# Kernel tuning notes

Hardware: AMD Instinct MI355X
Metric: run time of the kernel (lower is better)

The kernel has to match this reference:

```python
import jax, jax.numpy as jnp
import numpy as np

# ---- fixed configuration (see shape_source) ----
B, ND, NPR = 64, 32, 32          # batch, drug-subgraph nodes, protein-subgraph nodes
LD, LP = 100, 1000               # drug_MAX_LENGH, protein_MAX_LENGH
DIM, CONV = 64, 40               # char_dim, conv
DK, PK = (4, 6, 8), (4, 8, 12)   # drug_kernel, protein_kernel
VD, VP = 71, 26                  # SMILES / FASTA vocab sizes
ED, EP, EDP = 128, 128, 64       # DDI / PPI / DPI edges per subgraph
GNN_LAYERS = 2
SLOPE = 0.01                     # LeakyReLU default slope


def setup_inputs():
    key = jax.random.key(0)
    ks = iter(jax.random.split(key, 64))
    def nrm(shape, s=0.02):
        return jax.random.normal(next(ks), shape, jnp.float32) * s
    inp = {}
    inp['drug_tokens'] = jax.random.randint(next(ks), (B, LD), 0, VD, jnp.int32)
    inp['protein_tokens'] = jax.random.randint(next(ks), (B, LP), 0, VP, jnp.int32)
    inp['drug_node_tokens'] = jax.random.randint(next(ks), (B, ND, LD), 0, VD, jnp.int32)
    inp['protein_node_tokens'] = jax.random.randint(next(ks), (B, NPR, LP), 0, VP, jnp.int32)
    inp['ddi_edges'] = jax.random.randint(next(ks), (B, 2, ED), 0, ND, jnp.int32)
    inp['ppi_edges'] = jax.random.randint(next(ks), (B, 2, EP), 0, NPR, jnp.int32)
    inp['dpi_edges'] = jax.random.randint(next(ks), (B, 2, EDP), 0, min(ND, NPR), jnp.int32)
    # sequence embeddings (padding_idx=0 -> zero row)
    inp['drug_embed'] = nrm((VD, DIM)).at[0].set(0.)
    inp['protein_embed'] = nrm((VP, DIM)).at[0].set(0.)
    # drug CNN stack
    inp['dW1'], inp['db1'] = nrm((CONV, DIM, DK[0])), jnp.zeros((CONV,), jnp.float32)
    inp['dW2'], inp['db2'] = nrm((2*CONV, CONV, DK[1])), jnp.zeros((2*CONV,), jnp.float32)
    inp['dW3'], inp['db3'] = nrm((4*CONV, 2*CONV, DK[2])), jnp.zeros((4*CONV,), jnp.float32)
    # protein CNN stack
    inp['pW1'], inp['pb1'] = nrm((CONV, DIM, PK[0])), jnp.zeros((CONV,), jnp.float32)
    inp['pW2'], inp['pb2'] = nrm((2*CONV, CONV, PK[1])), jnp.zeros((2*CONV,), jnp.float32)
    inp['pW3'], inp['pb3'] = nrm((4*CONV, 2*CONV, PK[2])), jnp.zeros((4*CONV,), jnp.float32)
    # graph node-feature embedding tables (creat_drug_node / creat_protein_node)
    inp['drug_node_table'] = nrm((VD, LD)).at[0].set(0.)
    inp['protein_node_table'] = nrm((VP, LP)).at[0].set(0.)
    # SAGEConv params: Wl (neighbor path, has bias), Wr (root path, no bias)
    inp['ddi_Wl'], inp['ddi_bl'], inp['ddi_Wr'] = nrm((LD, LD)), jnp.zeros((LD,), jnp.float32), nrm((LD, LD))
    inp['ppi_Wl'], inp['ppi_bl'], inp['ppi_Wr'] = nrm((LP, LP)), jnp.zeros((LP,), jnp.float32), nrm((LP, LP))
    inp['dpi_Wl'], inp['dpi_bl'], inp['dpi_Wr'] = nrm((LP, LD)), jnp.zeros((LP,), jnp.float32), nrm((LP, LP))
    inp['pdi_Wl'], inp['pdi_bl'], inp['pdi_Wr'] = nrm((LD, LP)), jnp.zeros((LD,), jnp.float32), nrm((LD, LD))
    # fusion MLP
    inp['fc1_W'], inp['fc1_b'] = nrm((1024, 1420)), jnp.zeros((1024,), jnp.float32)
    inp['fc2_W'], inp['fc2_b'] = nrm((1024, 1024)), jnp.zeros((1024,), jnp.float32)
    inp['fc3_W'], inp['fc3_b'] = nrm((512, 1024)), jnp.zeros((512,), jnp.float32)
    inp['out_W'], inp['out_b'] = nrm((2, 512)), jnp.zeros((2,), jnp.float32)
    return inp


def _conv_relu(x, w, b):
    # x: [B, Cin, L], w: [Cout, Cin, K] -> valid Conv1d + ReLU
    y = jax.lax.conv_general_dilated(x, w, (1,), 'VALID',
                                     dimension_numbers=('NCH', 'OIH', 'NCH'))
    return jax.nn.relu(y + b[None, :, None])


def _node_feat(tokens, table, vocab):
    # mean over sequence of embedded tokens == (token-count histogram / L) @ table
    counts = jax.nn.one_hot(tokens, vocab, dtype=table.dtype).sum(axis=2)  # [B, N, V]
    return jnp.einsum('bnv,vd->bnd', counts, table) / tokens.shape[-1]


def _sage(xs, xd, edges, Wl, bl, Wr):
    # PyG SAGEConv, aggr='mean': lin_l(mean_j x_src[j]) + lin_r(x_dst)
    src, dst = edges[0], edges[1]
    n = xd.shape[0]
    s = jax.ops.segment_sum(xs[src], dst, num_segments=n)
    c = jax.ops.segment_sum(jnp.ones((src.shape[0],), xs.dtype), dst, num_segments=n)
    agg = s / jnp.maximum(c, 1.0)[:, None]
    return agg @ Wl.T + bl + xd @ Wr.T


def _forward(drug_tokens, protein_tokens, drug_node_tokens, protein_node_tokens,
             ddi_edges, ppi_edges, dpi_edges,
             drug_embed, protein_embed,
             dW1, db1, dW2, db2, dW3, db3,
             pW1, pb1, pW2, pb2, pW3, pb3,
             drug_node_table, protein_node_table,
             ddi_Wl, ddi_bl, ddi_Wr, ppi_Wl, ppi_bl, ppi_Wr,
             dpi_Wl, dpi_bl, dpi_Wr, pdi_Wl, pdi_bl, pdi_Wr,
             fc1_W, fc1_b, fc2_W, fc2_b, fc3_W, fc3_b, out_W, out_b):
    # --- CNN branches (maxpool kernel spans whole remaining length == global max) ---
    x = drug_embed[drug_tokens].transpose(0, 2, 1)            # [B, DIM, LD]
    for w, b in ((dW1, db1), (dW2, db2), (dW3, db3)):
        x = _conv_relu(x, w, b)
    drug_feat = x.max(axis=2)                                 # [B, 4*CONV]
    y = protein_embed[protein_tokens].transpose(0, 2, 1)      # [B, DIM, LP]
    for w, b in ((pW1, pb1), (pW2, pb2), (pW3, pb3)):
        y = _conv_relu(y, w, b)
    prot_feat = y.max(axis=2)                                 # [B, 4*CONV]
    # --- graph node features: mean over sequence of node-token embeddings ---
    dx = _node_feat(drug_node_tokens, drug_node_table, VD)    # [B, ND, LD]
    px = _node_feat(protein_node_tokens, protein_node_table, VP)  # [B, NPR, LP]
    # --- hetero SAGE message passing, aggr='mean' across relations ---
    def _hetero(dxi, pxi, ddi, ppi, dpi):
        pdi = dpi[::-1]
        d = 0.5 * (_sage(dxi, dxi, ddi, ddi_Wl, ddi_bl, ddi_Wr)
                   + _sage(pxi, dxi, pdi, pdi_Wl, pdi_bl, pdi_Wr))
        p = 0.5 * (_sage(pxi, pxi, ppi, ppi_Wl, ppi_bl, ppi_Wr)
                   + _sage(dxi, pxi, dpi, dpi_Wl, dpi_bl, dpi_Wr))
        return d, p
    hetero_b = jax.vmap(_hetero)
    for _ in range(GNN_LAYERS):
        dx, px = hetero_b(dx, px, ddi_edges, ppi_edges, dpi_edges)
    # node 0 of each subgraph is the query drug / protein
    graph_feat = jnp.concatenate([dx[:, 0], px[:, 0]], axis=-1)   # [B, LD+LP]
    # --- fusion MLP (dropout = identity at eval) ---
    pair = jnp.concatenate([drug_feat, prot_feat, graph_feat], axis=-1)  # [B, 1420]
    h = jax.nn.leaky_relu(pair @ fc1_W.T + fc1_b, SLOPE)
    h = jax.nn.leaky_relu(h @ fc2_W.T + fc2_b, SLOPE)
    h = jax.nn.leaky_relu(h @ fc3_W.T + fc3_b, SLOPE)
    return h @ out_W.T + out_b                                 # [B, 2]


def reference(drug_tokens, protein_tokens, drug_node_tokens, protein_node_tokens,
              ddi_edges, ppi_edges, dpi_edges,
              drug_embed, protein_embed,
              dW1, db1, dW2, db2, dW3, db3,
              pW1, pb1, pW2, pb2, pW3, pb3,
              drug_node_table, protein_node_table,
              ddi_Wl, ddi_bl, ddi_Wr, ppi_Wl, ppi_bl, ppi_Wr,
              dpi_Wl, dpi_bl, dpi_Wr, pdi_Wl, pdi_bl, pdi_Wr,
              fc1_W, fc1_b, fc2_W, fc2_b, fc3_W, fc3_b, out_W, out_b):
    return _forward(drug_tokens, protein_tokens, drug_node_tokens, protein_node_tokens,
                    ddi_edges, ppi_edges, dpi_edges,
                    drug_embed, protein_embed,
                    dW1, db1, dW2, db2, dW3, db3,
                    pW1, pb1, pW2, pb2, pW3, pb3,
                    drug_node_table, protein_node_table,
                    ddi_Wl, ddi_bl, ddi_Wr, ppi_Wl, ppi_bl, ppi_Wr,
                    dpi_Wl, dpi_bl, dpi_Wr, pdi_Wl, pdi_bl, pdi_Wr,
                    fc1_W, fc1_b, fc2_W, fc2_b, fc3_W, fc3_b, out_W, out_b)
```

## Files before the change

kernel.cpp:

```cpp
#include <hip/hip_runtime.h>
#include <hip/hip_bf16.h>


typedef __attribute__((ext_vector_type(8))) short short8;
typedef __attribute__((ext_vector_type(4))) float f32x4;
union FragU { uint32_t u[4]; uint4 q; short8 s; };

static __device__ inline unsigned short f2bf(float v) {
    __hip_bfloat16 h = __float2bfloat16(v);
    return *(unsigned short*)&h;
}

static constexpr size_t O_PAIR = 0;
static constexpr size_t O_CF1  = 363520;
static constexpr size_t O_CF2  = 625664;
static constexpr size_t O_CF3  = 887808;
static constexpr size_t O_BD   = 1018880;
static constexpr size_t O_BP   = 1019392;
static constexpr size_t O_WDS  = 1023488;
static constexpr size_t O_WPS  = 1342976;
static constexpr size_t O_WTP1 = 5864960;
static constexpr size_t O_WTP2 = 5930496;
static constexpr size_t O_WTP3 = 6012416;
static constexpr size_t O_WTD1 = 6503936;
static constexpr size_t O_WTD2 = 6569472;
static constexpr size_t O_WTD3 = 6651392;
static constexpr size_t AR     = 6897152;
static constexpr size_t A_AD  = AR + 0;
static constexpr size_t A_AP  = AR + 479232;
static constexpr size_t A_A2D = AR + 1327104;
static constexpr size_t A_A2P = AR + 1486848;
static constexpr size_t A_UD  = AR + 1769472;
static constexpr size_t A_UP  = AR + 1855488;
static constexpr size_t A_RHO = AR + 2641920;
static constexpr size_t A_Y2P = AR + 0;
static constexpr size_t A_Y1P = AR + 10158080;
static constexpr size_t A_Y1D = AR + 15278080;
static constexpr size_t A_Y2D = AR + 15810560;
static constexpr size_t NEED_BYTES = AR + 16793600;

__global__ void zero32_k(uint32_t* __restrict__ p, int n) {
    int i = blockIdx.x * 256 + threadIdx.x;
    if (i < n) p[i] = 0u;
}

static constexpr long Q0 = 100;
static constexpr long Q1 = Q0 + 1000;
static constexpr long Q2 = Q1 + 14336;
static constexpr long Q3 = Q2 + 14336;
static constexpr long Q4 = Q3 + 131072;
static constexpr long Q5 = Q4 + 1048576;
static constexpr long Q6 = Q5 + 1048576;
static constexpr long Q7 = Q6 + 163840;
static constexpr long Q8 = Q7 + 32768;
static constexpr long Q9 = Q8 + 40960;
static constexpr long Q10 = Q9 + 245760;
static constexpr long Q11 = Q10 + 32768;
static constexpr long Q12 = Q11 + 40960;
static constexpr long Q13 = Q12 + 122880;
static constexpr long Q14 = Q13 + 70400;
static constexpr long Q15 = Q14 + 20480;
static constexpr long Q16 = Q15 + 163840;
static constexpr long Q17 = Q16 + 660736;

__device__ inline void wt_block(unsigned short* dst, int ld_dst, int coloff,
                                const float* s1, const float* s2, int ld_src,
                                int N, int Kreal, int Kblk, long local) {
    int n = (int)(local / Kblk), k = (int)(local % Kblk);
    float v = 0.f;
    if (n < N && k < Kreal) {
        v = s1[(size_t)n * ld_src + k];
        if (s2) v += s2[(size_t)n * ld_src + k];
    }
    dst[(size_t)n * ld_dst + coloff + k] = f2bf(v);
}

__device__ inline void wtconv_block(unsigned short* dst, const float* W,
                                    int Co, int Ci, int K, int KP, long local) {
    int co = (int)(local / (Ci * KP));
    int rem = (int)(local % (Ci * KP));
    int ci = rem / KP, k = rem % KP;
    float v = (co < Co && k < K) ? W[((size_t)co * Ci + ci) * K + k] : 0.f;
    dst[local] = f2bf(v);
}

__global__ __launch_bounds__(256) void prep_k(
    float* bd, float* bp, unsigned short* WdS, unsigned short* WpS,
    unsigned short* WtP1, unsigned short* WtP2, unsigned short* WtP3,
    unsigned short* WtD1, unsigned short* WtD2, unsigned short* WtD3,
    float* pair, float* cfz, uint32_t* gnnz,
    const float* ddi_Wl, const float* ddi_bl, const float* ddi_Wr,
    const float* ppi_Wl, const float* ppi_bl, const float* ppi_Wr,
    const float* dpi_Wl, const float* dpi_bl, const float* dpi_Wr,
    const float* pdi_Wl, const float* pdi_bl, const float* pdi_Wr,
    const float* dW1, const float* dW2, const float* dW3,
    const float* pW1, const float* pW2, const float* pW3) {
    long idx = (long)blockIdx.x * 256 + threadIdx.x;
    if (idx < Q0) { bd[idx] = 0.5f * (ddi_bl[idx] + pdi_bl[idx]); return; }
    if (idx < Q1) { long j = idx - Q0; bp[j] = 0.5f * (ppi_bl[j] + dpi_bl[j]); return; }
    if (idx < Q2) { wt_block(WdS, 1248, 0, ddi_Wl, nullptr, 100, 100, 100, 112, idx - Q1); return; }
    if (idx < Q3) { wt_block(WdS, 1248, 112, ddi_Wr, pdi_Wr, 100, 100, 100, 112, idx - Q2); return; }
    if (idx < Q4) { wt_block(WdS, 1248, 224, pdi_Wl, nullptr, 1000, 100, 1000, 1024, idx - Q3); return; }
    if (idx < Q5) { wt_block(WpS, 2208, 0, ppi_Wl, nullptr, 1000, 1000, 1000, 1024, idx - Q4); return; }
    if (idx < Q6) { wt_block(WpS, 2208, 1024, ppi_Wr, dpi_Wr, 1000, 1000, 1000, 1024, idx - Q5); return; }
    if (idx < Q7) { wt_block(WpS, 2208, 2048, dpi_Wl, nullptr, 100, 1000, 100, 160, idx - Q6); return; }
    if (idx < Q8)  { wtconv_block(WtP1, pW1, 40, 64, 4, 8, idx - Q7); return; }
    if (idx < Q9)  { wtconv_block(WtP2, pW2, 80, 40, 8, 8, idx - Q8); return; }
    if (idx < Q10) { wtconv_block(WtP3, pW3, 160, 80, 12, 16, idx - Q9); return; }
    if (idx < Q11) { wtconv_block(WtD1, dW1, 40, 64, 4, 8, idx - Q10); return; }
    if (idx < Q12) { wtconv_block(WtD2, dW2, 80, 40, 6, 8, idx - Q11); return; }
    if (idx < Q13) { wtconv_block(WtD3, dW3, 160, 80, 8, 8, idx - Q12); return; }
    if (idx < Q14) {
        long l = idx - Q13;
        int b = (int)(l / 1100), j = (int)(l % 1100);
        if (j < 100) pair[(size_t)b * 1420 + 320 + j] = 0.5f * (ddi_bl[j] + pdi_bl[j]);
        else { int j2 = j - 100; pair[(size_t)b * 1420 + 420 + j2] = 0.5f * (ppi_bl[j2] + dpi_bl[j2]); }
        return;
    }
    if (idx < Q15) {
        long l = idx - Q14;
        int b = (int)(l / 320), j = (int)(l % 320);
        pair[(size_t)b * 1420 + j] = 0.f;
// ... 94 lines not shown
    float invL = 1.f / (float)L;
    for (int o = tid; o < 7 * V; o += 256) {
        int i = o / V, v = o % V;
        float a = 0.f;
        for (int k = 0; k < 32; ++k) a += W7[i][k] * (float)cnt[k][v];
        WC[i][v] = a * invL;
    }
    __syncthreads();
    size_t g0d = (size_t)b * 1248, g1d_ = (size_t)(64 + b) * 1248, g2d = (size_t)(128 + b) * 1248;
    size_t g0p = (size_t)b * 2208, g1p = (size_t)(64 + b) * 2208, g2p = (size_t)(128 + b) * 2208;
    if (role == 0) {
        int d = tid;
        if (d >= 100) return;
        float acc[7] = {};
        for (int v = 0; v < 71; ++v) {
            float tv = dtable[(size_t)v * 100 + d];
            #pragma unroll
            for (int i = 0; i < 7; ++i) acc[i] += WC[i][v] * tv;
        }
        unsigned short h;
        h = f2bf(acc[0]); Ad[g0d + d] = h;
        h = f2bf(acc[1]); Ad[g0d + 112 + d] = h; Ad[g1d_ + d] = h;
        h = f2bf(acc[2]); Ad[g1d_ + 112 + d] = h;
        h = f2bf(acc[3]); Ap[g0p + 2048 + d] = h;
        h = f2bf(acc[4]); Ap[g1p + 2048 + d] = h;
        h = f2bf(acc[5]); Ap[g2p + 2048 + d] = h; Ad[g2d + 112 + d] = h;
        h = f2bf(acc[6]); Ad[g2d + d] = h;
    } else {
        for (int d = tid; d < 1000; d += 256) {
            float acc[7] = {};
            for (int v = 0; v < 26; ++v) {
                float tv = ptable[(size_t)v * 1000 + d];
                #pragma unroll
                for (int i = 0; i < 7; ++i) acc[i] += WC[i][v] * tv;
            }
            unsigned short h;
            h = f2bf(acc[0]); Ad[g0d + 224 + d] = h;
            h = f2bf(acc[1]); Ad[g1d_ + 224 + d] = h; Ap[g0p + 1024 + d] = h;
            h = f2bf(acc[2]); Ap[g0p + d] = h;
            h = f2bf(acc[3]); Ap[g1p + d] = h;
            h = f2bf(acc[4]); Ap[g1p + 1024 + d] = h; Ap[g2p + d] = h;
            h = f2bf(acc[5]); Ap[g2p + 1024 + d] = h;
            h = f2bf(acc[6]); Ad[g2d + 224 + d] = h;
        }
    }
}

__device__ __forceinline__ void sk_body(const unsigned short* __restrict__ A, int lda,
                                        const unsigned short* __restrict__ Bm, int ldb,
                                        int K, int KS, float scale,
                                        float* __restrict__ out,
                                        int rs, int coloff, int Nw,
                                        int bx, int by, int gz) {
    const int tid = threadIdx.x;
    const int lane = tid & 63, w = tid >> 6, c = lane & 15, q = lane >> 4;
    const int n = bx * 64 + w * 16 + c;
    const unsigned short* Ab = A + (size_t)gz * 64 * lda;
    const int Ks = ((K / KS + 31) / 32) * 32;
    const int k0 = by * Ks;
    const int k1 = min(K, k0 + Ks);
    f32x4 acc[4];
    #pragma unroll
    for (int i = 0; i < 4; ++i) acc[i] = (f32x4){0.f, 0.f, 0.f, 0.f};
    for (int k = k0; k < k1; k += 32) {
        FragU bf;
        bf.q = *(const uint4*)&Bm[(size_t)n * ldb + k + q * 8];
        #pragma unroll
        for (int i = 0; i < 4; ++i) {
            FragU af;
            af.q = *(const uint4*)&Ab[(size_t)(i * 16 + c) * lda + k + q * 8];
            acc[i] = __builtin_amdgcn_mfma_f32_16x16x32_bf16(af.s, bf.s, acc[i], 0, 0, 0);
        }
    }
    if (n >= Nw) return;
    #pragma unroll
    for (int i = 0; i < 4; ++i)
        #pragma unroll
        for (int r = 0; r < 4; ++r) {
            int m = gz * 64 + i * 16 + q * 4 + r;
            atomicAdd(&out[(size_t)m * rs + coloff + n], scale * acc[i][r]);
        }
}

__global__ __launch_bounds__(256) void sk_stage1(const unsigned short* __restrict__ Ad,
                                                 const unsigned short* __restrict__ WdS,
                                                 float* __restrict__ Ud,
                                                 const unsigned short* __restrict__ Ap,
                                                 const unsigned short* __restrict__ WpS,
                                                 float* __restrict__ Up) {
    int z = blockIdx.z;
    if (z < 3) {
        sk_body(Ap, 2208, WpS, 2208, 2208, 8, 0.5f, Up, 1024, 0, 1000,
                blockIdx.x, blockIdx.y, z);
    } else {
        if (blockIdx.x >= 2) return;
        sk_body(Ad, 1248, WdS, 1248, 1248, 8, 0.5f, Ud, 112, 0, 100,
                blockIdx.x, blockIdx.y, z - 3);
    }
}

__global__ __launch_bounds__(256) void sk_stage2(const unsigned short* __restrict__ A2d,
                                                 const unsigned short* __restrict__ WdS,
                                                 const unsigned short* __restrict__ A2p,
                                                 const unsigned short* __restrict__ WpS,
                                                 float* __restrict__ pair) {
    int z = blockIdx.z;
    if (z == 0) {
        sk_body(A2p, 2208, WpS, 2208, 2208, 8, 0.5f, pair, 1420, 420, 1000,
                blockIdx.x, blockIdx.y, 0);
    } else {
        if (blockIdx.x >= 2) return;
        sk_body(A2d, 1248, WdS, 1248, 1248, 8, 0.5f, pair, 1420, 320, 100,
                blockIdx.x, blockIdx.y, 0);
    }
}

__global__ void ep_k(const float* __restrict__ Ud, const float* __restrict__ Up,
                     const float* __restrict__ RHO,
                     const float* __restrict__ bd, const float* __restrict__ bp,
                     unsigned short* __restrict__ A2d, unsigned short* __restrict__ A2p) {
    int idx = blockIdx.x * 256 + threadIdx.x;
    if (idx < 192 * 112) {
        int m = idx / 112, n = idx % 112;
        if (n >= 100) return;
        int g = m >> 6, b = m & 63;
        float rho = (g == 0) ? RHO[b * 4 + 0] : (g == 1) ? 1.f : RHO[b * 4 + 3];
        unsigned short h = f2bf(Ud[idx] + rho * bd[n]);
        if (g == 0) A2d[(size_t)b * 1248 + n] = h;
        else if (g == 1) A2d[(size_t)b * 1248 + 112 + n] = h;
        else A2p[(size_t)b * 2208 + 2048 + n] = h;
    } else {
        int l = idx - 192 * 112;
        if (l >= 192 * 1024) return;
        int m = l / 1024, n = l % 1024;
        if (n >= 1000) return;
        int g = m >> 6, b = m & 63;
        float rho = (g == 0) ? RHO[b * 4 + 1] : (g == 1) ? RHO[b * 4 + 2] : 1.f;
        unsigned short h = f2bf(Up[l] + rho * bp[n]);
        if (g == 0) A2d[(size_t)b * 1248 + 224 + n] = h;
        else if (g == 1) A2p[(size_t)b * 2208 + n] = h;
        else A2p[(size_t)b * 2208 + 1024 + n] = h;
    }
}

template <int KP>
__device__ __forceinline__ void conv_body(const unsigned short* __restrict__ xin,
                                          int Ci, int Lp,
                                          const unsigned short* __restrict__ Wt, int KK,
                                          int nchunk,
                                          const float* __restrict__ bias, int Co,
                                          unsigned short* __restrict__ yout,
                                          int Lout, int LoutPad,
                                          float* __restrict__ pool, int pool_coloff,
                                          int b, int co0, int t0,
                                          unsigned short* As, unsigned short* xraw) {
    constexpr int CIPC = 64 / KP;
    constexpr int LG = (KP == 8) ? 3 : 4;
    const int tid = threadIdx.x;
    const int lane = tid & 63, w = tid >> 6, c = lane & 15, q = lane >> 4;
    f32x4 acc[4][4];
    #pragma unroll
    for (int i = 0; i < 4; ++i)
        #pragma unroll
        for (int j = 0; j < 4; ++j) acc[i][j] = (f32x4){0.f, 0.f, 0.f, 0.f};
    const int row8 = tid >> 3, col8 = (tid & 7) * 8;
    for (int ch = 0; ch < nchunk; ++ch) {
        const int kkbase = ch * 64, ci0 = ch * CIPC;
        #pragma unroll
        for (int p = 0; p < 2; ++p) {
            int row = row8 + p * 32;
            *(uint4*)&As[row * 72 + col8] =
                *(const uint4*)&Wt[(size_t)(co0 + row) * KK + kkbase + col8];
        }
        for (int gi = tid; gi < CIPC * 34; gi += 256) {
            int ci = gi / 34, g8 = (gi % 34) * 8, gt = t0 + g8;
            const unsigned short* src = xin + ((size_t)b * Ci + ci0 + ci) * Lp + gt;
            if (gt + 8 <= Lp) {
                *(uint4*)&xraw[ci * 272 + g8] = *(const uint4*)src;
            } else {
                #pragma unroll
                for (int jj = 0; jj < 8; ++jj)
                    xraw[ci * 272 + g8 + jj] = (gt + jj < Lp) ? src[jj] : (unsigned short)0;
            }
        }
        __syncthreads();
        #pragma unroll
        for (int ks = 0; ks < 2; ++ks) {
            const int kc = ks * 32;
            FragU af[4];
            #pragma unroll
            for (int i = 0; i < 4; ++i)
                af[i].q = *(const uint4*)&As[(i * 16 + c) * 72 + kc + q * 8];
            const int koff = kc + q * 8;
            const int cioff = koff >> LG;
            const int k0 = koff & (KP - 1);
            const uint32_t* xr = (const uint32_t*)xraw + cioff * 136;
            #pragma unroll
            for (int j = 0; j < 4; ++j) {
                int tt = w * 64 + j * 16 + c;
                int eoff = tt + k0;
                int d0 = eoff >> 1;
                unsigned sh = (unsigned)(eoff & 1) * 16u;
                uint32_t u0 = xr[d0], u1 = xr[d0 + 1], u2 = xr[d0 + 2],
                         u3 = xr[d0 + 3], u4 = xr[d0 + 4];
                FragU bf;
                bf.u[0] = __builtin_amdgcn_alignbit(u1, u0, sh);
                bf.u[1] = __builtin_amdgcn_alignbit(u2, u1, sh);
                bf.u[2] = __builtin_amdgcn_alignbit(u3, u2, sh);
                bf.u[3] = __builtin_amdgcn_alignbit(u4, u3, sh);
                #pragma unroll
                for (int i = 0; i < 4; ++i)
                    acc[i][j] = __builtin_amdgcn_mfma_f32_16x16x32_bf16(af[i].s, bf.s,
                                                                        acc[i][j], 0, 0, 0);
            }
        }
        __syncthreads();
    }
    if (pool) {
        #pragma unroll
        for (int i = 0; i < 4; ++i) {
            #pragma unroll
            for (int r = 0; r < 4; ++r) {
                int co = co0 + i * 16 + q * 4 + r;
                float bv = (co < Co) ? bias[co] : 0.f;
                float v = 0.f;
                #pragma unroll
                for (int j = 0; j < 4; ++j) {
                    int t = t0 + w * 64 + j * 16 + c;
                    if (t < Lout) v = fmaxf(v, fmaxf(acc[i][j][r] + bv, 0.f));
                }
                v = fmaxf(v, __shfl_xor(v, 1));
                v = fmaxf(v, __shfl_xor(v, 2));
                v = fmaxf(v, __shfl_xor(v, 4));
                v = fmaxf(v, __shfl_xor(v, 8));
                if (c == 0 && co < Co)
                    atomicMax((int*)&pool[(size_t)b * 1420 + pool_coloff + co],
                              __float_as_int(v));
            }
        }
    } else {
        #pragma unroll
        for (int i = 0; i < 4; ++i) {
            #pragma unroll
            for (int r = 0; r < 4; ++r) {
                int co = co0 + i * 16 + q * 4 + r;
                if (co >= Co) continue;
                float bv = bias[co];
                #pragma unroll
                for (int j = 0; j < 4; ++j) {
                    int t = t0 + w * 64 + j * 16 + c;
                    if (t < Lout) {
                        yout[((size_t)b * Co + co) * LoutPad + t] =
                            f2bf(fmaxf(acc[i][j][r] + bv, 0.f));
                    } else if (t < LoutPad) {
                        yout[((size_t)b * Co + co) * LoutPad + t] = 0;
                    }
                }
            }
        }
    }
}

__device__ __forceinline__ void conv1e_body(const int* __restrict__ toks,
                                            const float* __restrict__ table, int V, int L,
                                            const unsigned short* __restrict__ Wt, int KK,
                                            const float* __restrict__ bias, int Co,
                                            unsigned short* __restrict__ yout,
                                            int Lout, int LoutPad,
                                            int b, int co0, int t0,
                                            unsigned short* As, unsigned short* xraw,
                                            unsigned short* tabT, int* tok_s) {
    const int tid = threadIdx.x;
    const int lane = tid & 63, w = tid >> 6, c = lane & 15, q = lane >> 4;
    for (int idx = tid; idx < 64 * V; idx += 256) {
        int ci = idx / V, v = idx % V;
        tabT[ci * 72 + v] = f2bf(table[(size_t)v * 64 + ci]);
    }
    for (int t = tid; t < 272; t += 256) {
        int gt = t0 + t;
        tok_s[t] = (gt < L) ? toks[(size_t)b * L + gt] : 0;
    }
    __syncthreads();
    f32x4 acc[4][4];
    #pragma unroll
    for (int i = 0; i < 4; ++i)
        #pragma unroll
        for (int j = 0; j < 4; ++j) acc[i][j] = (f32x4){0.f, 0.f, 0.f, 0.f};
    const int row8 = tid >> 3, col8 = (tid & 7) * 8;
    for (int ch = 0; ch < 8; ++ch) {
        const int kkbase = ch * 64, ci0 = ch * 8;
        #pragma unroll
        for (int p = 0; p < 2; ++p) {
            int row = row8 + p * 32;
            *(uint4*)&As[row * 72 + col8] =
                *(const uint4*)&Wt[(size_t)(co0 + row) * KK + kkbase + col8];
        }
        for (int gi = tid; gi < 8 * 272; gi += 256) {
            int ci = gi / 272, t = gi % 272;
            xraw[gi] = tabT[(ci0 + ci) * 72 + tok_s[t]];
        }
        __syncthreads();
        #pragma unroll
        for (int ks = 0; ks < 2; ++ks) {
            const int kc = ks * 32;
            FragU af[4];
            #pragma unroll
            for (int i = 0; i < 4; ++i)
                af[i].q = *(const uint4*)&As[(i * 16 + c) * 72 + kc + q * 8];
            const int koff = kc + q * 8;
            const int cioff = koff >> 3;
            const uint32_t* xr = (const uint32_t*)xraw + cioff * 136;
            #pragma unroll
            for (int j = 0; j < 4; ++j) {
                int tt = w * 64 + j * 16 + c;
                int d0 = tt >> 1;
                unsigned sh = (unsigned)(tt & 1) * 16u;
                uint32_t u0 = xr[d0], u1 = xr[d0 + 1], u2 = xr[d0 + 2],
                         u3 = xr[d0 + 3], u4 = xr[d0 + 4];
                FragU bf;
                bf.u[0] = __builtin_amdgcn_alignbit(u1, u0, sh);
                bf.u[1] = __builtin_amdgcn_alignbit(u2, u1, sh);
                bf.u[2] = __builtin_amdgcn_alignbit(u3, u2, sh);
                bf.u[3] = __builtin_amdgcn_alignbit(u4, u3, sh);
                #pragma unroll
                for (int i = 0; i < 4; ++i)
                    acc[i][j] = __builtin_amdgcn_mfma_f32_16x16x32_bf16(af[i].s, bf.s,
                                                                        acc[i][j], 0, 0, 0);
            }
        }
        __syncthreads();
    }
    #pragma unroll
    for (int i = 0; i < 4; ++i) {
        #pragma unroll
        for (int r = 0; r < 4; ++r) {
            int co = co0 + i * 16 + q * 4 + r;
            if (co >= Co) continue;
            float bv = bias[co];
            #pragma unroll
            for (int j = 0; j < 4; ++j) {
                int t = t0 + w * 64 + j * 16 + c;
                if (t < Lout) {
                    yout[((size_t)b * Co + co) * LoutPad + t] =
                        f2bf(fmaxf(acc[i][j][r] + bv, 0.f));
                } else if (t < LoutPad) {
                    yout[((size_t)b * Co + co) * LoutPad + t] = 0;
                }
            }
        }
    }
}

__global__ __launch_bounds__(256) void conv1_dual(
    const int* __restrict__ ptoks, const float* __restrict__ ptable,
    const unsigned short* __restrict__ WtP1, const float* __restrict__ pb1,
    unsigned short* __restrict__ y1p,
    const int* __restrict__ dtoks, const float* __restrict__ dtable,
    const unsigned short* __restrict__ WtD1, const float* __restrict__ db1,
    unsigned short* __restrict__ y1d) {
    __shared__ __align__(16) unsigned short As[64 * 72];
    __shared__ __align__(16) unsigned short xraw[8 * 272];
    __shared__ unsigned short tabT[64 * 72];
    __shared__ int tok_s[272];
    int z = blockIdx.z;
    if (z < 64) {
        conv1e_body(ptoks, ptable, 26, 1000, WtP1, 512, pb1, 40, y1p, 997, 1000,
                    z, 0, blockIdx.x * 256, As, xraw, tabT, tok_s);
    } else {
        if (blockIdx.x > 0) return;
        conv1e_body(dtoks, dtable, 71, 100, WtD1, 512, db1, 40, y1d, 97, 104,
                    z - 64, 0, 0, As, xraw, tabT, tok_s);
    }
}

__global__ __launch_bounds__(256) void conv2_dual(
    const unsigned short* __restrict__ y1p, const unsigned short* __restrict__ WtP2,
    const float* __restrict__ pb2, unsigned short* __restrict__ y2p,
    const unsigned short* __restrict__ y1d, const unsigned short* __restrict__ WtD2,
    const float* __restrict__ db2, unsigned short* __restrict__ y2d) {
    __shared__ __align__(16) unsigned short As[64 * 72];
    __shared__ __align__(16) unsigned short xraw[8 * 272];
    int z = blockIdx.z;
    if (z < 64) {
        conv_body<8>(y1p, 40, 1000, WtP2, 320, 5, pb2, 80, y2p, 990, 992,
                     nullptr, 0, z, blockIdx.y * 64, blockIdx.x * 256, As, xraw);
    } else {
        if (blockIdx.x > 0) return;
        conv_body<8>(y1d, 40, 104, WtD2, 320, 5, db2, 80, y2d, 92, 96,
                     nullptr, 0, z - 64, blockIdx.y * 64, 0, As, xraw);
    }
}

__global__ __launch_bounds__(256) void conv3_dual(
    const unsigned short* __restrict__ y2p, const unsigned short* __restrict__ WtP3,
    const float* __restrict__ pb3, float* __restrict__ pair,
    const unsigned short* __restrict__ y2d, const unsigned short* __restrict__ WtD3,
    const float* __restrict__ db3) {
    __shared__ __align__(16) unsigned short As[64 * 72];
    __shared__ __align__(16) unsigned short xraw[8 * 272];
    int z = blockIdx.z;
    if (z < 64) {
        conv_body<16>(y2p, 80, 992, WtP3, 1280, 20, pb3, 160, nullptr, 979, 0,
                      pair, 160, z, blockIdx.y * 64, blockIdx.x * 256, As, xraw);
    } else {
        if (blockIdx.x > 0) return;
        conv_body<8>(y2d, 80, 96, WtD3, 640, 10, db3, 160, nullptr, 85, 0,
                     pair, 0, z - 64, blockIdx.y * 64, 0, As, xraw);
    }
}

__global__ __launch_bounds__(256) void gemm_nt(const float* __restrict__ A, int lda,
                                               const float* __restrict__ Aep_b,
                                               const float* __restrict__ Bm,
                                               float* __restrict__ Cout,
                                               int M, int N, int K, int KC) {
    const int m0 = blockIdx.x * 64, n0 = blockIdx.y * 64, s = blockIdx.z;
    const int tid = threadIdx.x, ty = tid >> 4, tx = tid & 15;
    __shared__ __align__(16) float As[16][68];
    __shared__ __align__(16) float Bs[16][68];
    float acc[4][4] = {};
    const int kbeg = s * KC, kend = min(K, kbeg + KC);
    for (int k0 = kbeg; k0 < kend; k0 += 16) {
        int colk = k0 + tx;
        bool kok = colk < kend;
        #pragma unroll
        for (int qq = 0; qq < 4; ++qq) {
            int mi = ty + qq * 16;
            float va = 0.f;
            if (kok && (m0 + mi) < M) {
                va = A[(size_t)(m0 + mi) * lda + colk];
                if (Aep_b) {
                    va += Aep_b[colk];
                    va = va >= 0.f ? va : 0.01f * va;
                }
            }
            As[tx][mi] = va;
            Bs[tx][mi] = (kok && (n0 + mi) < N) ? Bm[(size_t)(n0 + mi) * K + colk] : 0.f;
        }
        __syncthreads();
        #pragma unroll
        for (int kk = 0; kk < 16; ++kk) {
            float4 a4 = *(const float4*)&As[kk][ty * 4];
            float4 b4 = *(const float4*)&Bs[kk][tx * 4];
            float av[4] = {a4.x, a4.y, a4.z, a4.w};
            float bv[4] = {b4.x, b4.y, b4.z, b4.w};
            #pragma unroll
            for (int i = 0; i < 4; ++i)
                #pragma unroll
                for (int j = 0; j < 4; ++j)
                    acc[i][j] = fmaf(av[i], bv[j], acc[i][j]);
        }
        __syncthreads();
    }
    #pragma unroll
    for (int i = 0; i < 4; ++i) {
        int m = m0 + ty * 4 + i;
        if (m >= M) continue;
        #pragma unroll
        for (int j = 0; j < 4; ++j) {
            int n = n0 + tx * 4 + j;
            if (n >= N) continue;
            atomicAdd(&Cout[(size_t)m * N + n], acc[i][j]);
        }
    }
}

__global__ void out_k(const float* __restrict__ cf3, const float* __restrict__ b3,
                      const float* __restrict__ W, const float* __restrict__ bias,
                      float* __restrict__ out) {
    int tid = threadIdx.x;
    if (tid >= 128) return;
    int b = tid >> 1, n = tid & 1;
    const float* hr = cf3 + (size_t)b * 512;
    const float* wr = W + (size_t)n * 512;
    float a = 0.f;
    for (int k = 0; k < 512; ++k) {
        float v = hr[k] + b3[k];
        v = v >= 0.f ? v : 0.01f * v;
        a = fmaf(v, wr[k], a);
    }
    out[b * 2 + n] = a + bias[n];
}

static inline int kc_of(int K, int S) { return ((K + S * 16 - 1) / (S * 16)) * 16; }
static inline dim3 g1d(int n) { return dim3((n + 255) / 256); }

extern "C" void kernel_launch(void* const* d_in, const int* in_sizes, int n_in,
                              void* d_out, int out_size, void* d_ws, size_t ws_size,
                              hipStream_t stream) {
    const int* drug_tokens       = (const int*)d_in[0];
    const int* protein_tokens    = (const int*)d_in[1];
    const int* drug_node_tokens  = (const int*)d_in[2];
    const int* protein_node_toks = (const int*)d_in[3];
    const int* ddi_edges         = (const int*)d_in[4];
    const int* ppi_edges         = (const int*)d_in[5];
    const int* dpi_edges         = (const int*)d_in[6];
    const float* drug_embed      = (const float*)d_in[7];
    const float* protein_embed   = (const float*)d_in[8];
    const float* dW1 = (const float*)d_in[9];  const float* db1 = (const float*)d_in[10];
    const float* dW2 = (const float*)d_in[11]; const float* db2 = (const float*)d_in[12];
    const float* dW3 = (const float*)d_in[13]; const float* db3 = (const float*)d_in[14];
    const float* pW1 = (const float*)d_in[15]; const float* pb1 = (const float*)d_in[16];
    const float* pW2 = (const float*)d_in[17]; const float* pb2 = (const float*)d_in[18];
    const float* pW3 = (const float*)d_in[19]; const float* pb3 = (const float*)d_in[20];
    const float* drug_node_table = (const float*)d_in[21];
    const float* prot_node_table = (const float*)d_in[22];
    const float* ddi_Wl = (const float*)d_in[23]; const float* ddi_bl = (const float*)d_in[24];
    const float* ddi_Wr = (const float*)d_in[25];
    const float* ppi_Wl = (const float*)d_in[26]; const float* ppi_bl = (const float*)d_in[27];
    const float* ppi_Wr = (const float*)d_in[28];
    const float* dpi_Wl = (const float*)d_in[29]; const float* dpi_bl = (const float*)d_in[30];
    const float* dpi_Wr = (const float*)d_in[31];
    const float* pdi_Wl = (const float*)d_in[32]; const float* pdi_bl = (const float*)d_in[33];
    const float* pdi_Wr = (const float*)d_in[34];
    const float* fc1_W = (const float*)d_in[35]; const float* fc1_b = (const float*)d_in[36];
    const float* fc2_W = (const float*)d_in[37]; const float* fc2_b = (const float*)d_in[38];
    const float* fc3_W = (const float*)d_in[39]; const float* fc3_b = (const float*)d_in[40];
    const float* out_W = (const float*)d_in[41]; const float* out_b = (const float*)d_in[42];

    float* outp = (float*)d_out;
    if (ws_size < NEED_BYTES) {
        zero32_k<<<g1d(out_size), 256, 0, stream>>>((uint32_t*)outp, out_size);
        return;
    }
    char* wsb = (char*)d_ws;
    float* pair = (float*)(wsb + O_PAIR);
    float* cf1 = (float*)(wsb + O_CF1); float* cf2 = (float*)(wsb + O_CF2);
    float* cf3 = (float*)(wsb + O_CF3);
    float* bd = (float*)(wsb + O_BD); float* bp = (float*)(wsb + O_BP);
    unsigned short* WdS  = (unsigned short*)(wsb + O_WDS);
    unsigned short* WpS  = (unsigned short*)(wsb + O_WPS);
    unsigned short* WtP1 = (unsigned short*)(wsb + O_WTP1);
    unsigned short* WtP2 = (unsigned short*)(wsb + O_WTP2);
    unsigned short* WtP3 = (unsigned short*)(wsb + O_WTP3);
    unsigned short* WtD1 = (unsigned short*)(wsb + O_WTD1);
    unsigned short* WtD2 = (unsigned short*)(wsb + O_WTD2);
    unsigned short* WtD3 = (unsigned short*)(wsb + O_WTD3);
    unsigned short* Ad  = (unsigned short*)(wsb + A_AD);
    unsigned short* Ap  = (unsigned short*)(wsb + A_AP);
    unsigned short* A2d = (unsigned short*)(wsb + A_A2D);
    unsigned short* A2p = (unsigned short*)(wsb + A_A2P);
    float* Ud  = (float*)(wsb + A_UD);
    float* Up  = (float*)(wsb + A_UP);
    float* RHO = (float*)(wsb + A_RHO);
    unsigned short* y2p = (unsigned short*)(wsb + A_Y2P);
    unsigned short* y1p = (unsigned short*)(wsb + A_Y1P);
    unsigned short* y1d = (unsigned short*)(wsb + A_Y1D);
    unsigned short* y2d = (unsigned short*)(wsb + A_Y2D);

    prep_k<<<g1d((int)Q17), 256, 0, stream>>>(bd, bp, WdS, WpS,
                                              WtP1, WtP2, WtP3, WtD1, WtD2, WtD3,
                                              pair, cf1, (uint32_t*)(wsb + A_AD),
                                              ddi_Wl, ddi_bl, ddi_Wr,
                                              ppi_Wl, ppi_bl, ppi_Wr,
                                              dpi_Wl, dpi_bl, dpi_Wr,
                                              pdi_Wl, pdi_bl, pdi_Wr,
                                              dW1, dW2, dW3, pW1, pW2, pW3);

    gnn_front_k<<<dim3(2, 64), 256, 0, stream>>>(ddi_edges, ppi_edges, dpi_edges,
                                                 drug_node_tokens, protein_node_toks,
                                                 drug_node_table, prot_node_table,
                                                 RHO, Ad, Ap);

    sk_stage1<<<dim3(16, 8, 6), 256, 0, stream>>>(Ad, WdS, Ud, Ap, WpS, Up);
    ep_k<<<g1d(192 * 112 + 192 * 1024), 256, 0, stream>>>(Ud, Up, RHO, bd, bp, A2d, A2p);
    sk_stage2<<<dim3(16, 8, 2), 256, 0, stream>>>(A2d, WdS, A2p, WpS, pair);

    conv1_dual<<<dim3(4, 1, 128), 256, 0, stream>>>(protein_tokens, protein_embed,
                                                    WtP1, pb1, y1p,
                                                    drug_tokens, drug_embed,
                                                    WtD1, db1, y1d);
    conv2_dual<<<dim3(4, 2, 128), 256, 0, stream>>>(y1p, WtP2, pb2, y2p,
                                                    y1d, WtD2, db2, y2d);
    conv3_dual<<<dim3(4, 3, 128), 256, 0, stream>>>(y2p, WtP3, pb3, pair,
                                                    y2d, WtD3, db3);

    gemm_nt<<<dim3(1, 16, 16), 256, 0, stream>>>(pair, 1420, nullptr, fc1_W, cf1,
                                                 64, 1024, 1420, kc_of(1420, 16));
    gemm_nt<<<dim3(1, 16, 16), 256, 0, stream>>>(cf1, 1024, fc1_b, fc2_W, cf2,
                                                 64, 1024, 1024, kc_of(1024, 16));
    gemm_nt<<<dim3(1, 8, 16), 256, 0, stream>>>(cf2, 1024, fc2_b, fc3_W, cf3,
                                                64, 512, 1024, kc_of(1024, 16));
    out_k<<<dim3(1), 128, 0, stream>>>(cf3, fc3_b, out_W, out_b, outp);
}
```

Before: 464.9 us.

## Merge GNN stages into conv launches and shrink conv time tiles

The GNN stage-1 GEMM now runs as extra blocks inside the conv2 launch, and the epilogue runs as extra blocks inside the conv3 launch, so independent work shares launches instead of running serially. The conv time tile is halved from 256 to 128 (JT=2), which doubles the block count to fill more CUs and cuts LDS use per block. When the workspace is large enough, the conv and GNN buffers no longer alias; otherwise a fallback path keeps the old serial order. The cost is heterogeneous blocks within one launch and more weight-tile reloads from the smaller tiles.

```diff
diff --git a/kernel.cpp b/kernel.cpp
--- a/kernel.cpp
+++ b/kernel.cpp
@@ -33,11 +33,13 @@
 static constexpr size_t A_UD  = AR + 1769472;
 static constexpr size_t A_UP  = AR + 1855488;
 static constexpr size_t A_RHO = AR + 2641920;
-static constexpr size_t A_Y2P = AR + 0;
-static constexpr size_t A_Y1P = AR + 10158080;
-static constexpr size_t A_Y1D = AR + 15278080;
-static constexpr size_t A_Y2D = AR + 15810560;
-static constexpr size_t NEED_BYTES = AR + 16793600;
+static constexpr size_t GNN_END = AR + 2642944;
+static constexpr size_t SZ_Y2P = 10158080;
+static constexpr size_t SZ_Y1P = 5120000;
+static constexpr size_t SZ_Y1D = 532480;
+static constexpr size_t SZ_Y2D = 983040;
+static constexpr size_t NEED_FB   = AR + SZ_Y2P + SZ_Y1P + SZ_Y1D + SZ_Y2D;
+static constexpr size_t NEED_FULL = GNN_END + SZ_Y2P + SZ_Y1P + SZ_Y1D + SZ_Y2D;
 
 __global__ void zero32_k(uint32_t* __restrict__ p, int n) {
     int i = blockIdx.x * 256 + threadIdx.x;
@@ -298,44 +300,10 @@
         }
 }
 
-__global__ __launch_bounds__(256) void sk_stage1(const unsigned short* __restrict__ Ad,
-                                                 const unsigned short* __restrict__ WdS,
-                                                 float* __restrict__ Ud,
-                                                 const unsigned short* __restrict__ Ap,
-                                                 const unsigned short* __restrict__ WpS,
-                                                 float* __restrict__ Up) {
-    int z = blockIdx.z;
-    if (z < 3) {
-        sk_body(Ap, 2208, WpS, 2208, 2208, 8, 0.5f, Up, 1024, 0, 1000,
-                blockIdx.x, blockIdx.y, z);
-    } else {
-        if (blockIdx.x >= 2) return;
-        sk_body(Ad, 1248, WdS, 1248, 1248, 8, 0.5f, Ud, 112, 0, 100,
-                blockIdx.x, blockIdx.y, z - 3);
-    }
-}
-
-__global__ __launch_bounds__(256) void sk_stage2(const unsigned short* __restrict__ A2d,
-                                                 const unsigned short* __restrict__ WdS,
-                                                 const unsigned short* __restrict__ A2p,
-                                                 const unsigned short* __restrict__ WpS,
-                                                 float* __restrict__ pair) {
-    int z = blockIdx.z;
-    if (z == 0) {
-        sk_body(A2p, 2208, WpS, 2208, 2208, 8, 0.5f, pair, 1420, 420, 1000,
-                blockIdx.x, blockIdx.y, 0);
-    } else {
-        if (blockIdx.x >= 2) return;
-        sk_body(A2d, 1248, WdS, 1248, 1248, 8, 0.5f, pair, 1420, 320, 100,
-                blockIdx.x, blockIdx.y, 0);
-    }
-}
-
-__global__ void ep_k(const float* __restrict__ Ud, const float* __restrict__ Up,
-                     const float* __restrict__ RHO,
-                     const float* __restrict__ bd, const float* __restrict__ bp,
-                     unsigned short* __restrict__ A2d, unsigned short* __restrict__ A2p) {
-    int idx = blockIdx.x * 256 + threadIdx.x;
+__device__ void ep_item(int idx, const float* __restrict__ Ud, const float* __restrict__ Up,
+                        const float* __restrict__ RHO,
+                        const float* __restrict__ bd, const float* __restrict__ bp,
+                        unsigned short* __restrict__ A2d, unsigned short* __restrict__ A2p) {
     if (idx < 192 * 112) {
         int m = idx / 112, n = idx % 112;
         if (n >= 100) return;
@@ -359,7 +327,7 @@
     }
 }
 
-template <int KP>
+template <int KP, int JT>
 __device__ __forceinline__ void conv_body(const unsigned short* __restrict__ xin,
                                           int Ci, int Lp,
                                           const unsigned short* __restrict__ Wt, int KK,
@@ -367,18 +335,20 @@
                                           const float* __restrict__ bias, int Co,
                                           unsigned short* __restrict__ yout,
                                           int Lout, int LoutPad,
-                                          float* __restrict__ pool, int pool_coloff,
+                                          float* __restrict__ pool_out, int pool_coloff,
                                           int b, int co0, int t0,
                                           unsigned short* As, unsigned short* xraw) {
     constexpr int CIPC = 64 / KP;
     constexpr int LG = (KP == 8) ? 3 : 4;
+    constexpr int WROW = JT * 64 + 16;
+    constexpr int NU4 = WROW / 8;
     const int tid = threadIdx.x;
     const int lane = tid & 63, w = tid >> 6, c = lane & 15, q = lane >> 4;
-    f32x4 acc[4][4];
+    f32x4 acc[4][JT];
     #pragma unroll
     for (int i = 0; i < 4; ++i)
         #pragma unroll
-        for (int j = 0; j < 4; ++j) acc[i][j] = (f32x4){0.f, 0.f, 0.f, 0.f};
+        for (int j = 0; j < JT; ++j) acc[i][j] = (f32x4){0.f, 0.f, 0.f, 0.f};
     const int row8 = tid >> 3, col8 = (tid & 7) * 8;
     for (int ch = 0; ch < nchunk; ++ch) {
         const int kkbase = ch * 64, ci0 = ch * CIPC;
@@ -388,15 +358,15 @@
             *(uint4*)&As[row * 72 + col8] =
                 *(const uint4*)&Wt[(size_t)(co0 + row) * KK + kkbase + col8];
         }
-        for (int gi = tid; gi < CIPC * 34; gi += 256) {
-            int ci = gi / 34, g8 = (gi % 34) * 8, gt = t0 + g8;
+        for (int gi = tid; gi < CIPC * NU4; gi += 256) {
+            int ci = gi / NU4, g8 = (gi % NU4) * 8, gt = t0 + g8;
             const unsigned short* src = xin + ((size_t)b * Ci + ci0 + ci) * Lp + gt;
             if (gt + 8 <= Lp) {
-                *(uint4*)&xraw[ci * 272 + g8] = *(const uint4*)src;
+                *(uint4*)&xraw[ci * WROW + g8] = *(const uint4*)src;
             } else {
                 #pragma unroll
                 for (int jj = 0; jj < 8; ++jj)
-                    xraw[ci * 272 + g8 + jj] = (gt + jj < Lp) ? src[jj] : (unsigned short)0;
+                    xraw[ci * WROW + g8 + jj] = (gt + jj < Lp) ? src[jj] : (unsigned short)0;
             }
         }
         __syncthreads();
@@ -410,10 +380,10 @@
             const int koff = kc + q * 8;
             const int cioff = koff >> LG;
             const int k0 = koff & (KP - 1);
-            const uint32_t* xr = (const uint32_t*)xraw + cioff * 136;
+            const uint32_t* xr = (const uint32_t*)xraw + cioff * (WROW / 2);
             #pragma unroll
-            for (int j = 0; j < 4; ++j) {
-                int tt = w * 64 + j * 16 + c;
+            for (int j = 0; j < JT; ++j) {
+                int tt = w * (JT * 16) + j * 16 + c;
                 int eoff = tt + k0;
                 int d0 = eoff >> 1;
                 unsigned sh = (unsigned)(eoff & 1) * 16u;
@@ -432,7 +402,7 @@
         }
         __syncthreads();
     }
-    if (pool) {
+    if (pool_out) {
         #pragma unroll
         for (int i = 0; i < 4; ++i) {
             #pragma unroll
@@ -441,8 +411,8 @@
                 float bv = (co < Co) ? bias[co] : 0.f;
                 float v = 0.f;
                 #pragma unroll
-                for (int j = 0; j < 4; ++j) {
-                    int t = t0 + w * 64 + j * 16 + c;
+                for (int j = 0; j < JT; ++j) {
+                    int t = t0 + w * (JT * 16) + j * 16 + c;
                     if (t < Lout) v = fmaxf(v, fmaxf(acc[i][j][r] + bv, 0.f));
                 }
                 v = fmaxf(v, __shfl_xor(v, 1));
@@ -450,7 +420,7 @@
                 v = fmaxf(v, __shfl_xor(v, 4));
                 v = fmaxf(v, __shfl_xor(v, 8));
                 if (c == 0 && co < Co)
-                    atomicMax((int*)&pool[(size_t)b * 1420 + pool_coloff + co],
+                    atomicMax((int*)&pool_out[(size_t)b * 1420 + pool_coloff + co],
                               __float_as_int(v));
             }
         }
@@ -463,8 +433,8 @@
                 if (co >= Co) continue;
                 float bv = bias[co];
                 #pragma unroll
-                for (int j = 0; j < 4; ++j) {
-                    int t = t0 + w * 64 + j * 16 + c;
+                for (int j = 0; j < JT; ++j) {
+                    int t = t0 + w * (JT * 16) + j * 16 + c;
                     if (t < Lout) {
                         yout[((size_t)b * Co + co) * LoutPad + t] =
                             f2bf(fmaxf(acc[i][j][r] + bv, 0.f));
@@ -486,22 +456,23 @@
                                             int b, int co0, int t0,
                                             unsigned short* As, unsigned short* xraw,
                                             unsigned short* tabT, int* tok_s) {
+    constexpr int WROW = 144;
     const int tid = threadIdx.x;
     const int lane = tid & 63, w = tid >> 6, c = lane & 15, q = lane >> 4;
     for (int idx = tid; idx < 64 * V; idx += 256) {
         int ci = idx / V, v = idx % V;
         tabT[ci * 72 + v] = f2bf(table[(size_t)v * 64 + ci]);
     }
-    for (int t = tid; t < 272; t += 256) {
+    for (int t = tid; t < WROW; t += 256) {
         int gt = t0 + t;
         tok_s[t] = (gt < L) ? toks[(size_t)b * L + gt] : 0;
     }
     __syncthreads();
-    f32x4 acc[4][4];
+    f32x4 acc[4][2];
     #pragma unroll
     for (int i = 0; i < 4; ++i)
         #pragma unroll
-        for (int j = 0; j < 4; ++j) acc[i][j] = (f32x4){0.f, 0.f, 0.f, 0.f};
+        for (int j = 0; j < 2; ++j) acc[i][j] = (f32x4){0.f, 0.f, 0.f, 0.f};
     const int row8 = tid >> 3, col8 = (tid & 7) * 8;
     for (int ch = 0; ch < 8; ++ch) {
         const int kkbase = ch * 64, ci0 = ch * 8;
@@ -511,8 +482,8 @@
             *(uint4*)&As[row * 72 + col8] =
                 *(const uint4*)&Wt[(size_t)(co0 + row) * KK + kkbase + col8];
         }
-        for (int gi = tid; gi < 8 * 272; gi += 256) {
-            int ci = gi / 272, t = gi % 272;
+        for (int gi = tid; gi < 8 * WROW; gi += 256) {
+            int ci = gi / WROW, t = gi % WROW;
             xraw[gi] = tabT[(ci0 + ci) * 72 + tok_s[t]];
         }
         __syncthreads();
@@ -525,10 +496,10 @@
                 af[i].q = *(const uint4*)&As[(i * 16 + c) * 72 + kc + q * 8];
             const int koff = kc + q * 8;
             const int cioff = koff >> 3;
-            const uint32_t* xr = (const uint32_t*)xraw + cioff * 136;
+            const uint32_t* xr = (const uint32_t*)xraw + cioff * (WROW / 2);
             #pragma unroll
-            for (int j = 0; j < 4; ++j) {
-                int tt = w * 64 + j * 16 + c;
+            for (int j = 0; j < 2; ++j) {
+                int tt = w * 32 + j * 16 + c;
                 int d0 = tt >> 1;
                 unsigned sh = (unsigned)(tt & 1) * 16u;
                 uint32_t u0 = xr[d0], u1 = xr[d0 + 1], u2 = xr[d0 + 2],
@@ -554,8 +525,8 @@
             if (co >= Co) continue;
             float bv = bias[co];
             #pragma unroll
-            for (int j = 0; j < 4; ++j) {
-                int t = t0 + w * 64 + j * 16 + c;
+            for (int j = 0; j < 2; ++j) {
+                int t = t0 + w * 32 + j * 16 + c;
                 if (t < Lout) {
                     yout[((size_t)b * Co + co) * LoutPad + t] =
                         f2bf(fmaxf(acc[i][j][r] + bv, 0.f));
@@ -575,13 +546,13 @@
     const unsigned short* __restrict__ WtD1, const float* __restrict__ db1,
     unsigned short* __restrict__ y1d) {
     __shared__ __align__(16) unsigned short As[64 * 72];
-    __shared__ __align__(16) unsigned short xraw[8 * 272];
+    __shared__ __align__(16) unsigned short xraw[8 * 144];
     __shared__ unsigned short tabT[64 * 72];
-    __shared__ int tok_s[272];
+    __shared__ int tok_s[144];
     int z = blockIdx.z;
     if (z < 64) {
         conv1e_body(ptoks, ptable, 26, 1000, WtP1, 512, pb1, 40, y1p, 997, 1000,
-                    z, 0, blockIdx.x * 256, As, xraw, tabT, tok_s);
+                    z, 0, blockIdx.x * 128, As, xraw, tabT, tok_s);
     } else {
         if (blockIdx.x > 0) return;
         conv1e_body(dtoks, dtable, 71, 100, WtD1, 512, db1, 40, y1d, 97, 104,
@@ -589,39 +560,81 @@
     }
 }
 
-__global__ __launch_bounds__(256) void conv2_dual(
+__global__ __launch_bounds__(256) void m2_k(int nconv,
     const unsigned short* __restrict__ y1p, const unsigned short* __restrict__ WtP2,
     const float* __restrict__ pb2, unsigned short* __restrict__ y2p,
     const unsigned short* __restrict__ y1d, const unsigned short* __restrict__ WtD2,
-    const float* __restrict__ db2, unsigned short* __restrict__ y2d) {
+    const float* __restrict__ db2, unsigned short* __restrict__ y2d,
+    const unsigned short* __restrict__ Ad, const unsigned short* __restrict__ WdS,
+    float* __restrict__ Ud,
+    const unsigned short* __restrict__ Ap, const unsigned short* __restrict__ WpS,
+    float* __restrict__ Up) {
     __shared__ __align__(16) unsigned short As[64 * 72];
-    __shared__ __align__(16) unsigned short xraw[8 * 272];
-    int z = blockIdx.z;
-    if (z < 64) {
-        conv_body<8>(y1p, 40, 1000, WtP2, 320, 5, pb2, 80, y2p, 990, 992,
-                     nullptr, 0, z, blockIdx.y * 64, blockIdx.x * 256, As, xraw);
+    __shared__ __align__(16) unsigned short xraw[8 * 144];
+    int id = blockIdx.x;
+    if (id < nconv) {
+        if (id < 1024) {
+            int b = id >> 4, r = id & 15;
+            conv_body<8, 2>(y1p, 40, 1000, WtP2, 320, 5, pb2, 80, y2p, 990, 992,
+                            nullptr, 0, b, (r >> 3) * 64, (r & 7) * 128, As, xraw);
+        } else {
+            int t = id - 1024;
+            conv_body<8, 2>(y1d, 40, 104, WtD2, 320, 5, db2, 80, y2d, 92, 96,
+                            nullptr, 0, t >> 1, (t & 1) * 64, 0, As, xraw);
+        }
     } else {
-        if (blockIdx.x > 0) return;
-        conv_body<8>(y1d, 40, 104, WtD2, 320, 5, db2, 80, y2d, 92, 96,
-                     nullptr, 0, z - 64, blockIdx.y * 64, 0, As, xraw);
-    }
-}
-
-__global__ __launch_bounds__(256) void conv3_dual(
+        int t = id - nconv;
+        int bx = t & 15, by = (t >> 4) & 7, bz = t >> 7;
+        if (bz < 3) {
+            sk_body(Ap, 2208, WpS, 2208, 2208, 8, 0.5f, Up, 1024, 0, 1000, bx, by, bz);
+        } else {
+            if (bx >= 2) return;
+            sk_body(Ad, 1248, WdS, 1248, 1248, 8, 0.5f, Ud, 112, 0, 100, bx, by, bz - 3);
+        }
+    }
+}
+
+__global__ __launch_bounds__(256) void m3_k(int nconv,
     const unsigned short* __restrict__ y2p, const unsigned short* __restrict__ WtP3,
     const float* __restrict__ pb3, float* __restrict__ pair,
     const unsigned short* __restrict__ y2d, const unsigned short* __restrict__ WtD3,
-    const float* __restrict__ db3) {
+    const float* __restrict__ db3,
+    const float* __restrict__ Ud, const float* __restrict__ Up,
+    const float* __restrict__ RHO,
+    const float* __restrict__ bd, const float* __restrict__ bp,
+    unsigned short* __restrict__ A2d, unsigned short* __restrict__ A2p) {
     __shared__ __align__(16) unsigned short As[64 * 72];
-    __shared__ __align__(16) unsigned short xraw[8 * 272];
+    __shared__ __align__(16) unsigned short xraw[8 * 144];
+    int id = blockIdx.x;
+    if (id < nconv) {
+        if (id < 1536) {
+            int b = id / 24, r = id % 24;
+            conv_body<16, 2>(y2p, 80, 992, WtP3, 1280, 20, pb3, 160, nullptr, 979, 0,
+                             pair, 160, b, (r >> 3) * 64, (r & 7) * 128, As, xraw);
+        } else {
+            int t = id - 1536;
+            conv_body<8, 2>(y2d, 80, 96, WtD3, 640, 10, db3, 160, nullptr, 85, 0,
+                            pair, 0, t / 3, (t % 3) * 64, 0, As, xraw);
+        }
+    } else {
+        int idx = (id - nconv) * 256 + threadIdx.x;
+        ep_item(idx, Ud, Up, RHO, bd, bp, A2d, A2p);
+    }
+}
+
+__global__ __launch_bounds__(256) void sk_stage2(const unsigned short* __restrict__ A2d,
+                                                 const unsigned short* __restrict__ WdS,
+                                                 const unsigned short* __restrict__ A2p,
+                                                 const unsigned short* __restrict__ WpS,
+                                                 float* __restrict__ pair) {
     int z = blockIdx.z;
-    if (z < 64) {
-        conv_body<16>(y2p, 80, 992, WtP3, 1280, 20, pb3, 160, nullptr, 979, 0,
-                      pair, 160, z, blockIdx.y * 64, blockIdx.x * 256, As, xraw);
+    if (z == 0) {
+        sk_body(A2p, 2208, WpS, 2208, 2208, 8, 0.5f, pair, 1420, 420, 1000,
+                blockIdx.x, blockIdx.y, 0);
     } else {
-        if (blockIdx.x > 0) return;
-        conv_body<8>(y2d, 80, 96, WtD3, 640, 10, db3, 160, nullptr, 85, 0,
-                     pair, 0, z - 64, blockIdx.y * 64, 0, As, xraw);
+        if (blockIdx.x >= 2) return;
+        sk_body(A2d, 1248, WdS, 1248, 1248, 8, 0.5f, pair, 1420, 320, 100,
+                blockIdx.x, blockIdx.y, 0);
     }
 }
 
@@ -735,10 +748,12 @@
     const float* out_W = (const float*)d_in[41]; const float* out_b = (const float*)d_in[42];
 
     float* outp = (float*)d_out;
-    if (ws_size < NEED_BYTES) {
+    if (ws_size < NEED_FB) {
         zero32_k<<<g1d(out_size), 256, 0, stream>>>((uint32_t*)outp, out_size);
         return;
     }
+    const bool full = (ws_size >= NEED_FULL);
+
     char* wsb = (char*)d_ws;
     float* pair = (float*)(wsb + O_PAIR);
     float* cf1 = (float*)(wsb + O_CF1); float* cf2 = (float*)(wsb + O_CF2);
@@ -759,10 +774,11 @@
     float* Ud  = (float*)(wsb + A_UD);
     float* Up  = (float*)(wsb + A_UP);
     float* RHO = (float*)(wsb + A_RHO);
-    unsigned short* y2p = (unsigned short*)(wsb + A_Y2P);
-    unsigned short* y1p = (unsigned short*)(wsb + A_Y1P);
-    unsigned short* y1d = (unsigned short*)(wsb + A_Y1D);
-    unsigned short* y2d = (unsigned short*)(wsb + A_Y2D);
+    size_t cbase = full ? GNN_END : AR;
+    unsigned short* y2p = (unsigned short*)(wsb + cbase);
+    unsigned short* y1p = (unsigned short*)(wsb + cbase + SZ_Y2P);
+    unsigned short* y1d = (unsigned short*)(wsb + cbase + SZ_Y2P + SZ_Y1P);
+    unsigned short* y2d = (unsigned short*)(wsb + cbase + SZ_Y2P + SZ_Y1P + SZ_Y1D);
 
     prep_k<<<g1d((int)Q17), 256, 0, stream>>>(bd, bp, WdS, WpS,
                                               WtP1, WtP2, WtP3, WtD1, WtD2, WtD3,
@@ -778,18 +794,31 @@
                                                  drug_node_table, prot_node_table,
                                                  RHO, Ad, Ap);
 
-    sk_stage1<<<dim3(16, 8, 6), 256, 0, stream>>>(Ad, WdS, Ud, Ap, WpS, Up);
-    ep_k<<<g1d(192 * 112 + 192 * 1024), 256, 0, stream>>>(Ud, Up, RHO, bd, bp, A2d, A2p);
-    sk_stage2<<<dim3(16, 8, 2), 256, 0, stream>>>(A2d, WdS, A2p, WpS, pair);
-
-    conv1_dual<<<dim3(4, 1, 128), 256, 0, stream>>>(protein_tokens, protein_embed,
-                                                    WtP1, pb1, y1p,
-                                                    drug_tokens, drug_embed,
-                                                    WtD1, db1, y1d);
-    conv2_dual<<<dim3(4, 2, 128), 256, 0, stream>>>(y1p, WtP2, pb2, y2p,
-                                                    y1d, WtD2, db2, y2d);
-    conv3_dual<<<dim3(4, 3, 128), 256, 0, stream>>>(y2p, WtP3, pb3, pair,
-                                                    y2d, WtD3, db3);
+    if (full) {
+        conv1_dual<<<dim3(8, 1, 128), 256, 0, stream>>>(protein_tokens, protein_embed,
+                                                        WtP1, pb1, y1p,
+                                                        drug_tokens, drug_embed,
+                                                        WtD1, db1, y1d);
+        m2_k<<<dim3(1152 + 768), 256, 0, stream>>>(1152,
+            y1p, WtP2, pb2, y2p, y1d, WtD2, db2, y2d, Ad, WdS, Ud, Ap, WpS, Up);
+        m3_k<<<dim3(1728 + 852), 256, 0, stream>>>(1728,
+            y2p, WtP3, pb3, pair, y2d, WtD3, db3, Ud, Up, RHO, bd, bp, A2d, A2p);
+        sk_stage2<<<dim3(16, 8, 2), 256, 0, stream>>>(A2d, WdS, A2p, WpS, pair);
+    } else {
+        m2_k<<<dim3(768), 256, 0, stream>>>(0,
+            y1p, WtP2, pb2, y2p, y1d, WtD2, db2, y2d, Ad, WdS, Ud, Ap, WpS, Up);
+        m3_k<<<dim3(852), 256, 0, stream>>>(0,
+            y2p, WtP3, pb3, pair, y2d, WtD3, db3, Ud, Up, RHO, bd, bp, A2d, A2p);
+        sk_stage2<<<dim3(16, 8, 2), 256, 0, stream>>>(A2d, WdS, A2p, WpS, pair);
+        conv1_dual<<<dim3(8, 1, 128), 256, 0, stream>>>(protein_tokens, protein_embed,
+                                                        WtP1, pb1, y1p,
+                                                        drug_tokens, drug_embed,
+                                                        WtD1, db1, y1d);
+        m2_k<<<dim3(1152), 256, 0, stream>>>(1152,
+            y1p, WtP2, pb2, y2p, y1d, WtD2, db2, y2d, Ad, WdS, Ud, Ap, WpS, Up);
+        m3_k<<<dim3(1728), 256, 0, stream>>>(1728,
+            y2p, WtP3, pb3, pair, y2d, WtD3, db3, Ud, Up, RHO, bd, bp, A2d, A2p);
+    }
 
     gemm_nt<<<dim3(1, 16, 16), 256, 0, stream>>>(pair, 1420, nullptr, fc1_W, cf1,
                                                  64, 1024, 1420, kc_of(1420, 16));
```

Result: faster. 441.8 us (-5.0%).
